# Kernel tuning notes

Measured on AMD Instinct MI355X. Metric: run time of the kernel, lower is better.

The kernel has to match this reference:

```python
import jax, jax.numpy as jnp
import numpy as np
from jax import lax

KERNEL = 31
SMOOTH = 0.001
PAD = KERNEL // 2


def _avg_pool2d(x):
    # torch F.avg_pool2d(kernel=31, stride=1, padding=15, count_include_pad=True):
    # sum over 31x31 window with zero padding, then divide by 31*31 always.
    s = lax.reduce_window(
        x, 0.0, lax.add,
        window_dimensions=(1, 1, KERNEL, KERNEL),
        window_strides=(1, 1, 1, 1),
        padding=((0, 0), (0, 0), (PAD, PAD), (PAD, PAD)),
    )
    return s / (KERNEL * KERNEL)


def setup_inputs() -> dict:
    key = jax.random.key(0)
    k1, k2 = jax.random.split(key)
    B, C, H, W = 32, 1, 1024, 1024
    output = jax.random.normal(k1, (B, C, H, W), dtype=jnp.float32)
    target = jax.random.uniform(k2, (B, C, H, W), dtype=jnp.float32)
    return {"output": output, "target": target}


def reference(output, target):
    out = jax.nn.sigmoid(output)
    weight = 1.0 + 5.0 * jnp.abs(_avg_pool2d(target) - target)  # [B,C,H,W]
    inter = jnp.sum(out * target * weight, axis=(2, 3)).reshape(-1, 1)      # [B*C,1]
    mask_sum = jnp.sum((target + out) * weight, axis=(2, 3)).reshape(-1, 1)  # [B*C,1]
    loss = 1.0 - (2.0 * inter + SMOOTH) / (mask_sum + SMOOTH)
    return jnp.mean(loss)
```

## Files before the change

kernel.cpp:

```cpp
#include <hip/hip_runtime.h>
#include <math.h>


namespace {
constexpr int Bn = 32;
constexpr int Hn = 1024;
constexpr int Wn = 1024;
constexpr int Rn = 15;
constexpr int TX = 256;
constexpr int YS = 64;
constexpr int NB = YS / 8;
constexpr int NCOL = TX + 32;
constexpr int PHYSW = (NCOL / 8) * 12;
constexpr float INV_KK = 1.0f / 961.0f;
}

__device__ __forceinline__ int phys(int i) { return i + ((i >> 3) << 2); }

__device__ __forceinline__ float ldcol(const float* p, int y, int col, bool xok) {
    return (xok && (unsigned)y < (unsigned)Hn) ? p[(size_t)y * Wn + col] : 0.0f;
}

__global__ __launch_bounds__(256, 4)
void dice_main(const float* __restrict__ logits, const float* __restrict__ tgt,
               float* __restrict__ acc)
{
    __shared__ __align__(16) float vbuf[8 * PHYSW];
    __shared__ float red[8];

    const int bid = blockIdx.x;
    const int b   = bid >> 6;
    const int rem = bid & 63;
    const int x0  = (rem >> 4) * TX;
    const int y0  = (rem & 15) * YS;
    const int t   = threadIdx.x;

    const float* tb = tgt    + (size_t)b * Hn * Wn;
    const float* ob = logits + (size_t)b * Hn * Wn;

    const int  col0 = x0 - Rn + t;
    const bool has2 = (t < 32);
    const int  col1 = col0 + 256;
    const bool xok0 = (col0 >= 0) && (col0 < Wn);
    const bool xok1 = (col1 >= 0) && (col1 < Wn);
    const int  pt   = phys(t);
    const int  pt2  = phys(256 + t);

    const int rr = t >> 5;
    const int jj = t & 31;
    const int xb = x0 + (jj << 3);

    float vs0 = 0.0f, vs1 = 0.0f;
    for (int yy = y0 - Rn; yy <= y0 + Rn; ++yy) {
        vs0 += ldcol(tb, yy, col0, xok0);
        if (has2) vs1 += ldcol(tb, yy, col1, xok1);
    }

    float pA[8], qA[8];
    #pragma unroll
    for (int r = 0; r < 8; ++r) {
        pA[r] = ldcol(tb, y0 + r + Rn, col0, xok0);
        qA[r] = has2 ? ldcol(tb, y0 + r + Rn, col1, xok1) : 0.0f;
    }
    float4 ct0, ct1, co0, co1;
    {
        const float* tp = tb + (size_t)(y0 + rr) * Wn + xb;
        const float* op = ob + (size_t)(y0 + rr) * Wn + xb;
        ct0 = ((const float4*)tp)[0]; ct1 = ((const float4*)tp)[1];
        co0 = ((const float4*)op)[0]; co1 = ((const float4*)op)[1];
    }

    float acc_i = 0.0f, acc_m = 0.0f;

    for (int it = 0; it < NB; ++it) {
        const int ya = y0 + it * 8;

        #pragma unroll
        for (int r = 0; r < 8; ++r) {
            const int yr = ya + r;
            if (it > 0 || r > 0) {
                vs0 += pA[r] - ldcol(tb, yr - Rn - 1, col0, xok0);
                if (has2) vs1 += qA[r] - ldcol(tb, yr - Rn - 1, col1, xok1);
            }
            vbuf[r * PHYSW + pt] = vs0;
            if (has2) vbuf[r * PHYSW + pt2] = vs1;
        }
        __syncthreads();

        float4 nt0, nt1, no0, no1;
        if (it + 1 < NB) {
            #pragma unroll
            for (int r = 0; r < 8; ++r) {
                pA[r] = ldcol(tb, ya + 8 + r + Rn, col0, xok0);
                if (has2) qA[r] = ldcol(tb, ya + 8 + r + Rn, col1, xok1);
            }
            const float* tp = tb + (size_t)(ya + 8 + rr) * Wn + xb;
            const float* op = ob + (size_t)(ya + 8 + rr) * Wn + xb;
            nt0 = ((const float4*)tp)[0]; nt1 = ((const float4*)tp)[1];
            no0 = ((const float4*)op)[0]; no1 = ((const float4*)op)[1];
        }

        {
            const float* vrow = &vbuf[rr * PHYSW];
            float w[40];
            #pragma unroll
            for (int k = 0; k < 10; ++k) {
                const float4 q = *(const float4*)&vrow[phys((jj << 3) + (k << 2))];
                w[4 * k + 0] = q.x; w[4 * k + 1] = q.y;
                w[4 * k + 2] = q.z; w[4 * k + 3] = q.w;
            }

            const float tc[8] = {ct0.x, ct0.y, ct0.z, ct0.w, ct1.x, ct1.y, ct1.z, ct1.w};
            const float oc[8] = {co0.x, co0.y, co0.z, co0.w, co1.x, co1.y, co1.z, co1.w};

            float s0 = 0.0f, s1 = 0.0f, s2 = 0.0f, s3 = 0.0f;
            #pragma unroll
            for (int c = 0; c < 28; c += 4) {
                s0 += w[c]; s1 += w[c + 1]; s2 += w[c + 2]; s3 += w[c + 3];
            }
            float s = (s0 + s1) + (s2 + s3) + w[28] + w[29] + w[30];
            #pragma unroll
            for (int m = 0; m < 8; ++m) {
                if (m > 0) s += w[30 + m] - w[m - 1];
                const float avg = s * INV_KK;
                const float wt  = 1.0f + 5.0f * fabsf(avg - tc[m]);
                const float sg  = 1.0f / (1.0f + __expf(-oc[m]));
                acc_i += sg * tc[m] * wt;
                acc_m += (tc[m] + sg) * wt;
            }
        }

        if (it + 1 < NB) { ct0 = nt0; ct1 = nt1; co0 = no0; co1 = no1; }
        __syncthreads();
    }

    #pragma unroll
    for (int off = 32; off > 0; off >>= 1) {
        acc_i += __shfl_down(acc_i, off);
        acc_m += __shfl_down(acc_m, off);
    }
    const int lane = t & 63;
    const int wv   = t >> 6;
    if (lane == 0) { red[wv * 2] = acc_i; red[wv * 2 + 1] = acc_m; }
    __syncthreads();
    if (t == 0) {
        atomicAdd(&acc[2 * b],     red[0] + red[2] + red[4] + red[6]);
        atomicAdd(&acc[2 * b + 1], red[1] + red[3] + red[5] + red[7]);
    }
}

__global__ void dice_final(const float* __restrict__ acc, float* __restrict__ out)
{
    const int t = threadIdx.x;
    float l = 0.0f;
    if (t < Bn) {
        const float I = acc[2 * t];
        const float M = acc[2 * t + 1];
        l = 1.0f - (2.0f * I + 0.001f) / (M + 0.001f);
    }
    #pragma unroll
    for (int off = 32; off > 0; off >>= 1) l += __shfl_down(l, off);
    if (t == 0) out[0] = l * (1.0f / 32.0f);
}

extern "C" void kernel_launch(void* const* d_in, const int* in_sizes, int n_in,
                              void* d_out, int out_size, void* d_ws, size_t ws_size,
                              hipStream_t stream)
{
    const float* logits = (const float*)d_in[0];
    const float* target = (const float*)d_in[1];
    float* acc = (float*)d_ws;

    hipMemsetAsync(d_ws, 0, 64 * sizeof(float), stream);
    dice_main<<<dim3(Bn * 64), dim3(256), 0, stream>>>(logits, target, acc);
    dice_final<<<dim3(1), dim3(64), 0, stream>>>(acc, (float*)d_out);
}
```

Baseline: 336.7 us.

## Drop register prefetch, shrink per-thread horizontal window to raise occupancy

Removes the software prefetch of the next 8 rows of column data and the center target/logit float4s, loading them inline instead. The horizontal window pass now gives each thread 4 outputs over two rows instead of 8 outputs in one row, which cuts the 40-float window array. Launch bounds go from 4 to 6 blocks per CU, and the x bounds checks are simplified to the one side that can fail. The goal is lower register pressure and higher occupancy so latency is hidden by more waves. The cost is losing explicit load/compute overlap and re-reading overlapping window data from LDS.

```diff
diff --git a/kernel.cpp b/kernel.cpp
--- a/kernel.cpp
+++ b/kernel.cpp
@@ -21,7 +21,7 @@
     return (xok && (unsigned)y < (unsigned)Hn) ? p[(size_t)y * Wn + col] : 0.0f;
 }
 
-__global__ __launch_bounds__(256, 4)
+__global__ __launch_bounds__(256, 6)
 void dice_main(const float* __restrict__ logits, const float* __restrict__ tgt,
                float* __restrict__ acc)
 {
@@ -41,33 +41,19 @@
     const int  col0 = x0 - Rn + t;
     const bool has2 = (t < 32);
     const int  col1 = col0 + 256;
-    const bool xok0 = (col0 >= 0) && (col0 < Wn);
-    const bool xok1 = (col1 >= 0) && (col1 < Wn);
+    const bool xok0 = (col0 >= 0);
+    const bool xok1 = (col1 < Wn);
     const int  pt   = phys(t);
     const int  pt2  = phys(256 + t);
 
-    const int rr = t >> 5;
-    const int jj = t & 31;
-    const int xb = x0 + (jj << 3);
+    const int r0 = t >> 6;
+    const int jj = t & 63;
+    const int xb = x0 + (jj << 2);
 
     float vs0 = 0.0f, vs1 = 0.0f;
     for (int yy = y0 - Rn; yy <= y0 + Rn; ++yy) {
         vs0 += ldcol(tb, yy, col0, xok0);
         if (has2) vs1 += ldcol(tb, yy, col1, xok1);
-    }
-
-    float pA[8], qA[8];
-    #pragma unroll
-    for (int r = 0; r < 8; ++r) {
-        pA[r] = ldcol(tb, y0 + r + Rn, col0, xok0);
-        qA[r] = has2 ? ldcol(tb, y0 + r + Rn, col1, xok1) : 0.0f;
-    }
-    float4 ct0, ct1, co0, co1;
-    {
-        const float* tp = tb + (size_t)(y0 + rr) * Wn + xb;
-        const float* op = ob + (size_t)(y0 + rr) * Wn + xb;
-        ct0 = ((const float4*)tp)[0]; ct1 = ((const float4*)tp)[1];
-        co0 = ((const float4*)op)[0]; co1 = ((const float4*)op)[1];
     }
 
     float acc_i = 0.0f, acc_m = 0.0f;
@@ -79,58 +65,51 @@
         for (int r = 0; r < 8; ++r) {
             const int yr = ya + r;
             if (it > 0 || r > 0) {
-                vs0 += pA[r] - ldcol(tb, yr - Rn - 1, col0, xok0);
-                if (has2) vs1 += qA[r] - ldcol(tb, yr - Rn - 1, col1, xok1);
+                vs0 += ldcol(tb, yr + Rn, col0, xok0) - ldcol(tb, yr - Rn - 1, col0, xok0);
+                if (has2) vs1 += ldcol(tb, yr + Rn, col1, xok1) - ldcol(tb, yr - Rn - 1, col1, xok1);
             }
             vbuf[r * PHYSW + pt] = vs0;
             if (has2) vbuf[r * PHYSW + pt2] = vs1;
         }
         __syncthreads();
 
-        float4 nt0, nt1, no0, no1;
-        if (it + 1 < NB) {
+        #pragma unroll
+        for (int ss = 0; ss < 2; ++ss) {
+            const int  row  = r0 + ss * 4;
+            const int  yrow = ya + row;
+            const float* vr = &vbuf[row * PHYSW];
+            const int  base = jj << 2;
+
+            const float4 tc4 = *(const float4*)(tb + (size_t)yrow * Wn + xb);
+            const float4 oc4 = *(const float4*)(ob + (size_t)yrow * Wn + xb);
+
+            const float4 a = *(const float4*)&vr[phys(base)];
+            float s = a.w;
             #pragma unroll
-            for (int r = 0; r < 8; ++r) {
-                pA[r] = ldcol(tb, ya + 8 + r + Rn, col0, xok0);
-                if (has2) qA[r] = ldcol(tb, ya + 8 + r + Rn, col1, xok1);
+            for (int k = 1; k < 7; ++k) {
+                const float4 q = *(const float4*)&vr[phys(base + 4 * k)];
+                s += (q.x + q.y) + (q.z + q.w);
             }
-            const float* tp = tb + (size_t)(ya + 8 + rr) * Wn + xb;
-            const float* op = ob + (size_t)(ya + 8 + rr) * Wn + xb;
-            nt0 = ((const float4*)tp)[0]; nt1 = ((const float4*)tp)[1];
-            no0 = ((const float4*)op)[0]; no1 = ((const float4*)op)[1];
-        }
+            const float4 h = *(const float4*)&vr[phys(base + 28)];
+            s += (h.x + h.y) + h.z;
+            const float4 g = *(const float4*)&vr[phys(base + 32)];
 
-        {
-            const float* vrow = &vbuf[rr * PHYSW];
-            float w[40];
+            float sm = s + (a.x + a.y) + a.z;
+            const float tcv[4]  = {tc4.x, tc4.y, tc4.z, tc4.w};
+            const float ocv[4]  = {oc4.x, oc4.y, oc4.z, oc4.w};
+            const float wsub[3] = {a.x, a.y, a.z};
+            const float wadd[3] = {h.w, g.x, g.y};
+
             #pragma unroll
-            for (int k = 0; k < 10; ++k) {
-                const float4 q = *(const float4*)&vrow[phys((jj << 3) + (k << 2))];
-                w[4 * k + 0] = q.x; w[4 * k + 1] = q.y;
-                w[4 * k + 2] = q.z; w[4 * k + 3] = q.w;
-            }
-
-            const float tc[8] = {ct0.x, ct0.y, ct0.z, ct0.w, ct1.x, ct1.y, ct1.z, ct1.w};
-            const float oc[8] = {co0.x, co0.y, co0.z, co0.w, co1.x, co1.y, co1.z, co1.w};
-
-            float s0 = 0.0f, s1 = 0.0f, s2 = 0.0f, s3 = 0.0f;
-            #pragma unroll
-            for (int c = 0; c < 28; c += 4) {
-                s0 += w[c]; s1 += w[c + 1]; s2 += w[c + 2]; s3 += w[c + 3];
-            }
-            float s = (s0 + s1) + (s2 + s3) + w[28] + w[29] + w[30];
-            #pragma unroll
-            for (int m = 0; m < 8; ++m) {
-                if (m > 0) s += w[30 + m] - w[m - 1];
-                const float avg = s * INV_KK;
-                const float wt  = 1.0f + 5.0f * fabsf(avg - tc[m]);
-                const float sg  = 1.0f / (1.0f + __expf(-oc[m]));
-                acc_i += sg * tc[m] * wt;
-                acc_m += (tc[m] + sg) * wt;
+            for (int m = 0; m < 4; ++m) {
+                if (m > 0) sm += wadd[m - 1] - wsub[m - 1];
+                const float avg = sm * INV_KK;
+                const float wt  = 1.0f + 5.0f * fabsf(avg - tcv[m]);
+                const float sg  = 1.0f / (1.0f + __expf(-ocv[m]));
+                acc_i += sg * tcv[m] * wt;
+                acc_m += (tcv[m] + sg) * wt;
             }
         }
-
-        if (it + 1 < NB) { ct0 = nt0; ct1 = nt1; co0 = no0; co1 = no1; }
         __syncthreads();
     }
 
```

Result: slower. 361.6 us (+7.4%).
